# Performance work log

Hardware: AMD Instinct MI355X
Metric: run time of the kernel (lower is better)

## Reference

```python
import jax, jax.numpy as jnp
import numpy as np

C = 256   # embedding_dim
B = 16
N = 2048
BN_EPS = 1e-5


def _sa_params(key, c):
    ks = jax.random.split(key, 8)
    s = 1.0 / np.sqrt(c)
    return dict(
        Wq=jax.random.normal(ks[0], (c // 2, c), jnp.float32) * s,
        Wk=jax.random.normal(ks[1], (c // 2, c), jnp.float32) * s,
        Wv=jax.random.normal(ks[2], (c, c), jnp.float32) * s,
        bv=jax.random.normal(ks[3], (c,), jnp.float32) * 0.01,
        Wt=jax.random.normal(ks[4], (c, c), jnp.float32) * s,
        bt=jax.random.normal(ks[5], (c,), jnp.float32) * 0.01,
        gamma=jnp.ones((c,), jnp.float32),
        beta=jnp.zeros((c,), jnp.float32),
    )


def setup_inputs() -> dict:
    key = jax.random.key(0)
    kx, k1, k2 = jax.random.split(key, 3)
    inp = {"x": jax.random.normal(kx, (B, C, N), jnp.float32)}
    for tag, kk in (("1", k1), ("2", k2)):
        for name, v in _sa_params(kk, C).items():
            inp[name + tag] = v
    return inp


def _sa_layer(x, Wq, Wk, Wv, bv, Wt, bt, gamma, beta):
    # 1x1 conv == per-point linear: [B,C,N]
    x_q = jnp.einsum('oc,bcn->bno', Wq, x)            # [B,N,C/2]
    x_k = jnp.einsum('oc,bcn->bon', Wk, x)            # [B,C/2,N]
    x_v = jnp.einsum('oc,bcn->bon', Wv, x) + bv[None, :, None]
    energy = jnp.einsum('bnc,bcm->bnm', x_q, x_k)     # [B,N,N]
    attn = jax.nn.softmax(energy, axis=-1)
    # offset-attention column-wise L1 renorm
    attn = attn / (1e-9 + attn.sum(axis=1, keepdims=True))
    x_r = jnp.einsum('bcn,bnm->bcm', x_v, attn)       # [B,C,N]
    h = x - x_r
    h = jnp.einsum('oc,bcn->bon', Wt, h) + bt[None, :, None]
    # BatchNorm1d (training mode, biased var over batch+points per channel)
    mean = h.mean(axis=(0, 2), keepdims=True)
    var = jnp.mean((h - mean) ** 2, axis=(0, 2), keepdims=True)
    h = (h - mean) * jax.lax.rsqrt(var + BN_EPS)
    h = h * gamma[None, :, None] + beta[None, :, None]
    return x + jax.nn.relu(h)


def reference(x,
              Wq1, Wk1, Wv1, bv1, Wt1, bt1, gamma1, beta1,
              Wq2, Wk2, Wv2, bv2, Wt2, bt2, gamma2, beta2):
    x1 = _sa_layer(x, Wq1, Wk1, Wv1, bv1, Wt1, bt1, gamma1, beta1)
    x2 = _sa_layer(x1, Wq2, Wk2, Wv2, bv2, Wt2, bt2, gamma2, beta2)
    return jnp.concatenate((x1, x2), axis=1)          # [B,2C,N]
```

## Files before the change

kernel.cpp:

```cpp
#include <hip/hip_runtime.h>

#define DI __device__ __forceinline__

typedef _Float16 f16_t;
typedef _Float16 f16x8 __attribute__((ext_vector_type(8)));
typedef float    f32x4 __attribute__((ext_vector_type(4)));

static_assert(sizeof(f16x8) == 16, "f16x8 must be 16B");

#define B_  16
#define C_  256
#define CH_ 128
#define N_  2048

DI f32x4 fzero(){ f32x4 z = {0.f,0.f,0.f,0.f}; return z; }
DI f16x8 ldg8(const f16_t* p){ return *(const f16x8*)p; }
DI f32x4 mfma16(f16x8 a, f16x8 b, f32x4 c){
  return __builtin_amdgcn_mfma_f32_16x16x32_f16(a, b, c, 0, 0, 0);
}
DI void split2(float v, f16_t& hi, f16_t& lo){
  hi = (f16_t)v; lo = (f16_t)(v - (float)hi);
}
DI int swz_b(int i){ return ((i&7)<<1) | ((i>>3)&1); }

#define GLL16(src, dst) __builtin_amdgcn_global_load_lds( \
    (const __attribute__((address_space(1))) void*)(src), \
    (__attribute__((address_space(3))) void*)(dst), 16, 0, 0)

__global__ void k_wconv(const float* q1,const float* k1,const float* v1,const float* t1,
                        const float* q2,const float* k2,const float* v2,const float* t2,
                        f16_t* out){
  int i = blockIdx.x*256 + threadIdx.x;
  int l = (i >= 196608) ? 1 : 0;
  int r = i - l*196608;
  const float* s; long dbase;
  if(r < 32768){ s = l? q2:q1; dbase = 0; }
  else if(r < 65536){ r -= 32768; s = l? k2:k1; dbase = 65536; }
  else if(r < 131072){ r -= 65536; s = l? v2:v1; dbase = 131072; }
  else { r -= 131072; s = l? t2:t1; dbase = 262144; }
  int o = r >> 8, c = r & 255;
  float v = s[o*256 + c];
  f16_t hi, lo; split2(v, hi, lo);
  f16_t* d = out + (long)l*393216 + dbase + (long)o*512;
  d[c] = hi; d[c+256] = lo;
}

__global__ void k_transpose(const float* __restrict__ X, long bstride,
                            f16_t* __restrict__ XtS){
  int b = blockIdx.x, n0 = blockIdx.y*32, c0 = blockIdx.z*64;
  __shared__ float tl[32][65];
  int t = threadIdx.x;
  int nn = t & 31, cr = t >> 5;
  const float* src = X + (long)b*bstride + n0 + nn;
  #pragma unroll
  for(int i=0;i<8;i++){
    int cc = cr + i*8;
    tl[nn][cc] = src[(long)(c0+cc)*N_];
  }
  __syncthreads();
  int n2 = t >> 3, cq = (t & 7)*8;
  __align__(16) f16_t hi8[8], lo8[8];
  #pragma unroll
  for(int j=0;j<8;j++) split2(tl[n2][cq+j], hi8[j], lo8[j]);
  f16_t* dst = XtS + ((long)b*N_ + n0 + n2)*512 + c0 + cq;
  *(f16x8*)dst         = *(f16x8*)hi8;
  *(f16x8*)(dst + 256) = *(f16x8*)lo8;
}

template<int LGX, int SPLIT_OUT, int BIAS, int DUAL>
__global__ __launch_bounds__(256) void k_gemm3(
    const f16_t* __restrict__ A, long sA,
    const f16_t* __restrict__ Bt, long sB,
    f16_t* __restrict__ out, int ldo, long sO,
    const float* __restrict__ bias, long dualoff)
{
  int i = blockIdx.x;
  int b = swz_b(i);
  int r = i>>4;
  int m0 = (r & ((1<<LGX)-1))*64, n0 = (r >> LGX)*64;
  int t = threadIdx.x, w = t>>6, l = t&63, lr = l&15, lg = l>>4;
  const f16_t* Ab = A + (long)b*sA + (long)(m0 + w*16 + lr)*512;
  const f16_t* Bb = Bt + (long)b*sB;
  f32x4 acc[4];
  #pragma unroll
  for(int i2=0;i2<4;i2++) acc[i2] = fzero();
  for(int k=0;k<256;k+=32){
    f16x8 ah = ldg8(Ab + k + lg*8);
    f16x8 al = ldg8(Ab + 256 + k + lg*8);
    #pragma unroll
    for(int ns=0;ns<4;ns++){
      const f16_t* brow = Bb + (long)(n0 + ns*16 + lr)*512;
      f16x8 bh = ldg8(brow + k + lg*8);
      f16x8 bl = ldg8(brow + 256 + k + lg*8);
      acc[ns] = mfma16(ah, bh, acc[ns]);
      acc[ns] = mfma16(ah, bl, acc[ns]);
      acc[ns] = mfma16(al, bh, acc[ns]);
    }
  }
  f16_t* ob = out + (long)b*sO;
  #pragma unroll
  for(int ns=0;ns<4;ns++){
    #pragma unroll
    for(int j=0;j<4;j++){
      int row = m0 + w*16 + lg*4 + j;
      int col = n0 + ns*16 + lr;
      float v = acc[ns][j];
      if(BIAS) v += bias[row];
      if(SPLIT_OUT){
        f16_t hi, lo; split2(v, hi, lo);
        f16_t* base = ob;
        if(DUAL && col >= 128) base = ob + (dualoff - 128);
        base[(long)row*ldo + col]       = hi;
        base[(long)row*ldo + col + 128] = lo;
      } else {
        ob[(long)row*ldo + col] = (f16_t)v;
      }
    }
  }
}

template<int T3>
__global__ __launch_bounds__(512) void k_rowstats(
    const f16_t* __restrict__ xqS, const f16_t* __restrict__ xkS,
    float* __restrict__ rowoff)
{
  extern __shared__ __align__(16) char smem[];
  const int bi = blockIdx.x;
  const int b = swz_b(bi);
  const int n0 = (bi>>4)*128;
  const int t = threadIdx.x, w = t>>6, l = t&63, lr = l&15, lg = l>>4;

  const f16_t* qp = xqS + ((long)b*N_ + n0 + w*16 + lr)*256;
  f16x8 bqh[4], bql[4];
  #pragma unroll
  for(int k=0;k<4;k++){
    bqh[k] = ldg8(qp + k*32 + lg*8);
    bql[k] = ldg8(qp + 128 + k*32 + lg*8);
  }
  const f16_t* kb = xkS + (long)b*N_*256;

  const int krow_off = l>>5, kslot = l&31;
  const f16_t *ks0, *ks1;
  { int row0 = w*2 + krow_off;
    ks0 = kb + (long)row0*256 + ((kslot ^ (row0&15))*8);
    int row1 = 16 + w*2 + krow_off;
    ks1 = kb + (long)row1*256 + ((kslot ^ (row1&15))*8); }

  #define KSTAGE(buf) do { char* kd = smem + (buf)*16384;                     \
    GLL16(ks0, kd + w*1024); GLL16(ks1, kd + 8192 + w*1024); } while(0)

  float rmax = -3e38f, rsum = 0.f;
  KSTAGE(0);

  #pragma unroll 1
  for(int i=0; i<64; i++){
    const int cur = i&1, nxt = cur^1;
    if(i<63){
      ks0 += 8192; ks1 += 8192;
      KSTAGE(nxt);
      asm volatile("s_waitcnt vmcnt(2)" ::: "memory");
    } else {
      asm volatile("s_waitcnt vmcnt(0)" ::: "memory");
    }
    asm volatile("s_barrier" ::: "memory");
    const char* kbuf = smem + cur*16384;
    #pragma unroll
    for(int s=0;s<2;s++){
      const char* krow = kbuf + (s*16 + lr)*512;
      f16x8 ah[4];
      #pragma unroll
      for(int k=0;k<4;k++)
        ah[k] = *(const f16x8*)(krow + ((((4*k+lg) ^ lr))<<4));
      f32x4 a1 = fzero(), a2 = fzero(), a3 = fzero();
      #pragma unroll
      for(int k=0;k<4;k++) a1 = mfma16(ah[k],  bqh[k], a1);
      #pragma unroll
      for(int k=0;k<4;k++) a2 = mfma16(ah[k],  bql[k], a2);
      if(T3){
        #pragma unroll
        for(int k=0;k<4;k++){
          f16x8 alk = *(const f16x8*)(krow + ((16 + (((4*k+lg)) ^ lr))<<4));
          a3 = mfma16(alk, bqh[k], a3);
        }
      }
      f32x4 acc = (a1 + a2) + a3;
      float vm = fmaxf(fmaxf(acc[0],acc[1]), fmaxf(acc[2],acc[3]));
      float nm = fmaxf(rmax, vm);
      rsum = rsum*__expf(rmax-nm)
           + __expf(acc[0]-nm)+__expf(acc[1]-nm)+__expf(acc[2]-nm)+__expf(acc[3]-nm);
      rmax = nm;
    }
    asm volatile("s_barrier" ::: "memory");
  }
  #undef KSTAGE

  #pragma unroll
  for(int off=16; off<64; off<<=1){
    float om = __shfl_xor(rmax, off, 64);
    float os = __shfl_xor(rsum, off, 64);
    float nm = fmaxf(rmax, om);
    rsum = rsum*__expf(rmax-nm) + os*__expf(om-nm);
    rmax = nm;
  }
  if(lg==0) rowoff[(long)b*N_ + n0 + w*16 + lr] = rmax + __logf(rsum);
}

__global__ __launch_bounds__(256) void k_apply(
    const f16_t* __restrict__ xqS, const f16_t* __restrict__ xkS,
    const f16_t* __restrict__ xv, const float* __restrict__ rowoff,
    const float* __restrict__ X, long xbstride, f16_t* __restrict__ h0T)
{
  extern __shared__ __align__(16) char smem[];
  const int bi = blockIdx.x;
  const int b = swz_b(bi);
  const int m0 = (bi>>4)*64;
  const int t = threadIdx.x, w = t>>6, l = t&63, lr = l&15, lg = l>>4;
  float* ro_s = (float*)(smem + 65536);
  {
    const float* rob = rowoff + (long)b*N_;
    *(f32x4*)(ro_s + t*4)        = *(const f32x4*)(rob + t*4);
    *(f32x4*)(ro_s + t*4 + 1024) = *(const f32x4*)(rob + t*4 + 1024);
  }

  const f16_t* akp = xkS + ((long)b*N_ + m0 + w*16 + lr)*256;
  f16x8 akh[4], akl[4];
  #pragma unroll
  for(int k=0;k<4;k++){
    akh[k] = ldg8(akp + k*32 + lg*8);
    akl[k] = ldg8(akp + 128 + k*32 + lg*8);
  }

  const f16_t* xqb = xqS + (long)b*N_*256;
  const f16_t* xvb = xv + (long)b*C_*N_;
  const int qperm = ((lr>>2)*8 + (lr&3));

  const int qrow_off = (l>>5), qslot = l&31;
  const int vc_off = (l>>2), vslot = l&3;

  const f16_t *qs0,*qs1,*qs2,*qs3,*vs0,*vs1,*vs2,*vs3;
  #define PINIT(r) { int qrow=(r*4+w)*2+qrow_off;                             \
    int qsw=(qrow&3)|(((qrow>>3)&3)<<2);                                      \
    qs##r = xqb + (long)qrow*256 + ((qslot ^ qsw)*8);                         \
    int vc=(r*4+w)*16+vc_off;                                                 \
    vs##r = xvb + (long)vc*N_ + ((vslot ^ (vc&3))*8); }
  PINIT(0) PINIT(1) PINIT(2) PINIT(3)
  #undef PINIT
  #define STAGE(buf) do {                                                     \
    char* qd = smem + (buf)*16384;                                            \
    char* vd = smem + 32768 + (buf)*16384;                                    \
    GLL16(qs0, qd + (0*4+w)*1024); GLL16(vs0, vd + (0*4+w)*1024);             \
    GLL16(qs1, qd + (1*4+w)*1024); GLL16(vs1, vd + (1*4+w)*1024);             \
    GLL16(qs2, qd + (2*4+w)*1024); GLL16(vs2, vd + (2*4+w)*1024);             \
    GLL16(qs3, qd + (3*4+w)*1024); GLL16(vs3, vd + (3*4+w)*1024); } while(0)
  #define PADV() do { qs0+=8192; qs1+=8192; qs2+=8192; qs3+=8192;             \
    vs0+=32; vs1+=32; vs2+=32; vs3+=32; } while(0)

  f32x4 y[16];
  #pragma unroll
  for(int i2=0;i2<16;i2++) y[i2] = fzero();
  float cs = 0.f, cm = -3e38f;

  __syncthreads();
  STAGE(0);

  const int vsl = (lg ^ (lr&3)) << 4;

  #pragma unroll 1
  for(int i=0; i<64; i++){
    const int cur = i&1, nxt = cur^1;
    const int n0 = i*32;
    if(i<63){
      PADV();
      STAGE(nxt);
      asm volatile("s_waitcnt vmcnt(8)" ::: "memory");
    } else {
      asm volatile("s_waitcnt vmcnt(0)" ::: "memory");
    }
    asm volatile("s_barrier" ::: "memory");
    const char* qb = smem + cur*16384;
    const char* vb = smem + 32768 + cur*16384;
    float g[2][4];
    #pragma unroll
    for(int s2=0;s2<2;s2++){
      const int rl = qperm + s2*4;
      const char* qrow = qb + rl*512;
      f16x8 qh[4], ql[4];
      #pragma unroll
      for(int k=0;k<4;k++){
        qh[k] = *(const f16x8*)(qrow + (((4*k + lg) ^ lr)<<4));
        ql[k] = *(const f16x8*)(qrow + 256 + (((4*k + lg) ^ lr)<<4));
      }
      f32x4 e1 = fzero(), e2 = fzero(), e3 = fzero();
      #pragma unroll
      for(int k=0;k<4;k++) e1 = mfma16(qh[k], akh[k], e1);
      #pragma unroll
      for(int k=0;k<4;k++) e2 = mfma16(ql[k], akh[k], e2);
      #pragma unroll
      for(int k=0;k<4;k++) e3 = mfma16(qh[k], akl[k], e3);
      f32x4 e = (e1 + e2) + e3;
      f32x4 ro4 = *(const f32x4*)(ro_s + n0 + lg*8 + s2*4);
      #pragma unroll
      for(int j=0;j<4;j++) g[s2][j] = e[j] - ro4[j];
    }
    float vl = fmaxf(fmaxf(fmaxf(g[0][0],g[0][1]), fmaxf(g[0][2],g[0][3])),
                     fmaxf(fmaxf(g[1][0],g[1][1]), fmaxf(g[1][2],g[1][3])));
    if(__any(vl > cm + 8.f)){
      float v = vl;
      v = fmaxf(v, __shfl_xor(v, 16, 64));
      v = fmaxf(v, __shfl_xor(v, 32, 64));
      bool need = v > cm + 8.f;
      if(need){
        float fj = __expf(cm - v);
        cm = v;
        cs *= fj;
        #pragma unroll
        for(int cf=0;cf<16;cf++){
          #pragma unroll
          for(int j2=0;j2<4;j2++) y[cf][j2] *= fj;
        }
      }
    }
    __align__(16) f16_t pv[8];
    #pragma unroll
    for(int s2=0;s2<2;s2++){
      #pragma unroll
      for(int j=0;j<4;j++){
        float p = __expf(g[s2][j] - cm);
        f16_t pb = (f16_t)p;
        cs += (float)pb;
        pv[s2*4+j] = pb;
      }
    }
    f16x8 pfrag = *(const f16x8*)pv;
    #pragma unroll
    for(int cf=0;cf<16;cf++){
      f16x8 av = *(const f16x8*)(vb + (cf*16 + lr)*64 + vsl);
      y[cf] = mfma16(av, pfrag, y[cf]);
    }
    asm volatile("s_barrier" ::: "memory");
  }
  #undef STAGE
  #undef PADV

  cs += __shfl_xor(cs, 16, 64);
  cs += __shfl_xor(cs, 32, 64);
  float inv = 1.f/(1e-9f*__expf(-cm) + cs);

  f16_t* H = (f16_t*)(smem + 49152);
  const int mq = t&63, cq = t>>6;
  const float* Xb = X + (long)b*xbstride + m0;
  uint4* dstb = (uint4*)(h0T + ((long)b*N_ + m0)*C_);
  #pragma unroll
  for(int half=0; half<2; half++){
    #pragma unroll
    for(int cf8=0; cf8<8; cf8++){
      int cf = half*8 + cf8;
      #pragma unroll
      for(int j=0;j<4;j++){
        int cl = cf8*16 + lg*4 + j;
        int m  = w*16 + lr;
        *(f16_t*)((char*)H + m*256 + ((((cl>>3) ^ (m&7))<<4) | ((cl&7)<<1)))
          = (f16_t)(y[cf][j]*inv);
      }
    }
    __syncthreads();
    #pragma unroll 4
    for(int ci=0; ci<32; ci++){
      int cl = cq*32 + ci;
      int c  = half*128 + cl;
      f16_t* hp = (f16_t*)((char*)H + mq*256 + ((((cl>>3) ^ (mq&7))<<4) | ((cl&7)<<1)));
      *hp = (f16_t)(Xb[(long)c*N_ + mq] - (float)*hp);
    }
    __syncthreads();
    {
      const uint4* src = (const uint4*)H;
      for(int i2=t;i2<1024;i2+=256){
        int row = i2>>4, slot = i2&15;
        dstb[row*32 + half*16 + slot] = src[(i2 & ~15) | (slot ^ (row&7))];
      }
    }
    __syncthreads();
  }
}

__global__ __launch_bounds__(256) void k_wt_bn(
    const f16_t* __restrict__ WtS, const f16_t* __restrict__ h0T,
    const float* __restrict__ bt,
    f16_t* __restrict__ h1, float* __restrict__ bnacc)
{
  int i = blockIdx.x;
  int b = swz_b(i);
  int r = i>>4;
  int o0 = (r&3)*64, m0 = (r>>2)*64;
  int t=threadIdx.x, w=t>>6, l=t&63, lr=l&15, lg=l>>4;
  const f16_t* Arow = WtS + (long)(o0 + w*16 + lr)*512;
  const f16_t* Bb = h0T + (long)b*N_*C_;
  f32x4 acc[4];
  #pragma unroll
  for(int i2=0;i2<4;i2++) acc[i2] = fzero();
  for(int k=0;k<C_;k+=32){
    f16x8 afh = ldg8(Arow + k + lg*8);
    f16x8 afl = ldg8(Arow + 256 + k + lg*8);
    #pragma unroll
    for(int ms=0;ms<4;ms++){
      f16x8 bf_ = ldg8(Bb + (long)(m0 + ms*16 + lr)*C_ + k + lg*8);
      acc[ms] = mfma16(afh, bf_, acc[ms]);
      acc[ms] = mfma16(afl, bf_, acc[ms]);
    }
  }
  float s1[4]={0.f,0.f,0.f,0.f}, s2v[4]={0.f,0.f,0.f,0.f};
  f16_t* h1b = h1 + (long)b*C_*N_;
  #pragma unroll
  for(int j=0;j<4;j++){
    int o = o0 + w*16 + lg*4 + j;
    float bias = bt[o];
    #pragma unroll
    for(int ms=0;ms<4;ms++){
      float v = acc[ms][j] + bias;
      h1b[(long)o*N_ + m0 + ms*16 + lr] = (f16_t)v;
      s1[j] += v; s2v[j] += v*v;
    }
  }
  #pragma unroll
  for(int off=1; off<16; off<<=1){
    #pragma unroll
    for(int j=0;j<4;j++){ s1[j]+=__shfl_xor(s1[j],off,64); s2v[j]+=__shfl_xor(s2v[j],off,64); }
  }
  if(lr==0){
    #pragma unroll
    for(int j=0;j<4;j++){
      int o = o0 + w*16 + lg*4 + j;
      atomicAdd(&bnacc[o], s1[j]);
      atomicAdd(&bnacc[256+o], s2v[j]);
    }
  }
}

__global__ void k_out(const f16_t* __restrict__ h1, const float* __restrict__ X, long xbstride,
                      const float* __restrict__ bnacc, const float* __restrict__ gamma,
                      const float* __restrict__ beta, float* __restrict__ out, long ocoff){
  long i = (long)blockIdx.x*256 + threadIdx.x;
  long e = i*8;
  int b = (int)(e >> 19);
  int rem = (int)(e & 524287);
  int c = rem >> 11;
  float mean = bnacc[c] * (1.f/32768.f);
  float var  = bnacc[256+c] * (1.f/32768.f) - mean*mean;
  float sc = gamma[c] * rsqrtf(var + 1e-5f);
  float sh = beta[c] - mean*sc;
  f16x8 hv = *(const f16x8*)(h1 + e);
  const float* xb = X + (long)b*xbstride + rem;
  float4 xr0 = *(const float4*)xb;
  float4 xr1 = *(const float4*)(xb + 4);
  float4 o0, o1;
  o0.x = xr0.x + fmaxf(fmaf((float)hv[0], sc, sh), 0.f);
  o0.y = xr0.y + fmaxf(fmaf((float)hv[1], sc, sh), 0.f);
  o0.z = xr0.z + fmaxf(fmaf((float)hv[2], sc, sh), 0.f);
  o0.w = xr0.w + fmaxf(fmaf((float)hv[3], sc, sh), 0.f);
  o1.x = xr1.x + fmaxf(fmaf((float)hv[4], sc, sh), 0.f);
  o1.y = xr1.y + fmaxf(fmaf((float)hv[5], sc, sh), 0.f);
  o1.z = xr1.z + fmaxf(fmaf((float)hv[6], sc, sh), 0.f);
  o1.w = xr1.w + fmaxf(fmaf((float)hv[7], sc, sh), 0.f);
  float* ob = out + (long)b*(512L*N_) + ocoff + rem;
  *(float4*)ob       = o0;
  *(float4*)(ob + 4) = o1;
}

extern "C" void kernel_launch(void* const* d_in, const int* in_sizes, int n_in,
                              void* d_out, int out_size, void* d_ws, size_t ws_size,
                              hipStream_t stream){
  (void)in_sizes; (void)n_in; (void)out_size; (void)ws_size;
  const float* x = (const float*)d_in[0];
  const float *Wf[2][4], *bv[2], *bt[2], *gm[2], *bb[2];
  for(int l=0;l<2;l++){
    int base = 1 + l*8;
    Wf[l][0]=(const float*)d_in[base+0];
    Wf[l][1]=(const float*)d_in[base+1];
    Wf[l][2]=(const float*)d_in[base+2];
    bv[l]   =(const float*)d_in[base+3];
    Wf[l][3]=(const float*)d_in[base+4];
    bt[l]   =(const float*)d_in[base+5];
    gm[l]   =(const float*)d_in[base+6];
    bb[l]   =(const float*)d_in[base+7];
  }
  char* ws = (char*)d_ws;
  size_t off = 0;
  auto alloc = [&](size_t bytes){ size_t o = off; off += (bytes + 255) & ~(size_t)255; return o; };
  size_t oXt = alloc((size_t)B_*N_*512*2);
  size_t oXq = alloc((size_t)B_*N_*256*2);
  size_t oXk = alloc((size_t)B_*N_*256*2);
  size_t oXv = alloc((size_t)B_*C_*N_*2);
  size_t oH0 = alloc((size_t)B_*N_*C_*2);
  size_t oRo = alloc((size_t)B_*N_*4);
  size_t oBn = alloc(2*512*4);
  size_t oW  = alloc((size_t)786432*2);

  hipMemsetAsync(ws + oBn, 0, 2*512*4, stream);
  k_wconv<<<1536,256,0,stream>>>(Wf[0][0],Wf[0][1],Wf[0][2],Wf[0][3],
                                 Wf[1][0],Wf[1][1],Wf[1][2],Wf[1][3],
                                 (f16_t*)(ws+oW));
  float* dout = (float*)d_out;
  f16_t* H1 = (f16_t*)(ws + oXq);
  const long XKOFF = ((long)(oXk - oXq)) / 2;
  for(int l=0;l<2;l++){
    const float* Xl = l ? dout : x;
    long xbs = l ? 512L*N_ : 256L*N_;
    const f16_t* WqS = (const f16_t*)(ws+oW) + (size_t)l*393216;
    const f16_t* WvS = WqS + 131072;
    const f16_t* WtS = WqS + 262144;
    f16_t* XtS = (f16_t*)(ws+oXt);
    f16_t* Xq  = (f16_t*)(ws+oXq);
    f16_t* Xk  = (f16_t*)(ws+oXk);
    f16_t* Xv  = (f16_t*)(ws+oXv);
    f16_t* H0  = (f16_t*)(ws+oH0);
    float* Ro  = (float*)(ws+oRo);
    float* Bn  = (float*)(ws+oBn) + l*512;

    k_transpose<<<dim3(B_, N_/32, C_/64),256,0,stream>>>(Xl, xbs, XtS);
    k_gemm3<5,1,0,1><<<2048,256,0,stream>>>(XtS, (long)N_*512, WqS, 0L,
                                            Xq, 256, (long)N_*256, nullptr, XKOFF);
    k_gemm3<2,0,1,0><<<2048,256,0,stream>>>(WvS, 0L, XtS, (long)N_*512,
                                            Xv, N_, (long)C_*N_, bv[l], 0L);
    if(l==0) k_rowstats<1><<<256,512,32768,stream>>>(Xq, Xk, Ro);
    else     k_rowstats<0><<<256,512,32768,stream>>>(Xq, Xk, Ro);
    k_apply<<<512,256,73728,stream>>>(Xq, Xk, Xv, Ro, Xl, xbs, H0);
    k_wt_bn<<<2048,256,0,stream>>>(WtS, H0, bt[l], H1, Bn);
    k_out<<<4096,256,0,stream>>>(H1, Xl, xbs, Bn, gm[l], bb[l], dout, (long)l*C_*N_);
  }
}
```

Before: 856.8 us.

## Double k_apply block to 512 threads covering 128 columns to share staged Q/V tiles

k_apply now runs 512-thread blocks, each handling 128 output columns instead of 64, with half as many blocks. The per-iteration Q and V tiles staged into shared memory are shared by eight waves instead of four, so each thread issues fewer global-to-LDS loads. Global traffic for the repeated xq/xv streams per batch drops by half. In exchange, the grid shrinks to 256 blocks, which lowers the number of independent blocks available to fill the GPU. The epilogue buffer is moved to a different LDS offset to fit the larger H tile.

```diff
diff --git a/kernel.cpp b/kernel.cpp
--- a/kernel.cpp
+++ b/kernel.cpp
@@ -205,7 +205,7 @@
   if(lg==0) rowoff[(long)b*N_ + n0 + w*16 + lr] = rmax + __logf(rsum);
 }
 
-__global__ __launch_bounds__(256) void k_apply(
+__global__ __launch_bounds__(512) void k_apply(
     const f16_t* __restrict__ xqS, const f16_t* __restrict__ xkS,
     const f16_t* __restrict__ xv, const float* __restrict__ rowoff,
     const float* __restrict__ X, long xbstride, f16_t* __restrict__ h0T)
@@ -213,13 +213,12 @@
   extern __shared__ __align__(16) char smem[];
   const int bi = blockIdx.x;
   const int b = swz_b(bi);
-  const int m0 = (bi>>4)*64;
+  const int m0 = (bi>>4)*128;
   const int t = threadIdx.x, w = t>>6, l = t&63, lr = l&15, lg = l>>4;
   float* ro_s = (float*)(smem + 65536);
   {
     const float* rob = rowoff + (long)b*N_;
-    *(f32x4*)(ro_s + t*4)        = *(const f32x4*)(rob + t*4);
-    *(f32x4*)(ro_s + t*4 + 1024) = *(const f32x4*)(rob + t*4 + 1024);
+    *(f32x4*)(ro_s + t*4) = *(const f32x4*)(rob + t*4);
   }
 
   const f16_t* akp = xkS + ((long)b*N_ + m0 + w*16 + lr)*256;
@@ -237,23 +236,20 @@
   const int qrow_off = (l>>5), qslot = l&31;
   const int vc_off = (l>>2), vslot = l&3;
 
-  const f16_t *qs0,*qs1,*qs2,*qs3,*vs0,*vs1,*vs2,*vs3;
-  #define PINIT(r) { int qrow=(r*4+w)*2+qrow_off;                             \
-    int qsw=(qrow&3)|(((qrow>>3)&3)<<2);                                      \
-    qs##r = xqb + (long)qrow*256 + ((qslot ^ qsw)*8);                         \
-    int vc=(r*4+w)*16+vc_off;                                                 \
-    vs##r = xvb + (long)vc*N_ + ((vslot ^ (vc&3))*8); }
-  PINIT(0) PINIT(1) PINIT(2) PINIT(3)
-  #undef PINIT
-  #define STAGE(buf) do {                                                     \
+  #define STAGE(nn, buf) do {                                                 \
     char* qd = smem + (buf)*16384;                                            \
     char* vd = smem + 32768 + (buf)*16384;                                    \
-    GLL16(qs0, qd + (0*4+w)*1024); GLL16(vs0, vd + (0*4+w)*1024);             \
-    GLL16(qs1, qd + (1*4+w)*1024); GLL16(vs1, vd + (1*4+w)*1024);             \
-    GLL16(qs2, qd + (2*4+w)*1024); GLL16(vs2, vd + (2*4+w)*1024);             \
-    GLL16(qs3, qd + (3*4+w)*1024); GLL16(vs3, vd + (3*4+w)*1024); } while(0)
-  #define PADV() do { qs0+=8192; qs1+=8192; qs2+=8192; qs3+=8192;             \
-    vs0+=32; vs1+=32; vs2+=32; vs3+=32; } while(0)
+    _Pragma("unroll")                                                         \
+    for(int r=0;r<2;r++){                                                     \
+      int qrow = (r*8+w)*2 + qrow_off;                                        \
+      int qsw  = (qrow&3) | (((qrow>>3)&3)<<2);                               \
+      const f16_t* qsrc = xqb + (long)((nn) + qrow)*256 + ((qslot ^ qsw)*8);  \
+      GLL16(qsrc, qd + (r*8+w)*1024);                                         \
+      int vc = (r*8+w)*16 + vc_off;                                           \
+      const f16_t* vsrc2 = xvb + (long)vc*N_ + (nn) + ((vslot ^ (vc&3))*8);   \
+      GLL16(vsrc2, vd + (r*8+w)*1024);                                        \
+    }                                                                         \
+  } while(0)
 
   f32x4 y[16];
   #pragma unroll
@@ -261,7 +257,7 @@
   float cs = 0.f, cm = -3e38f;
 
   __syncthreads();
-  STAGE(0);
+  STAGE(0, 0);
 
   const int vsl = (lg ^ (lr&3)) << 4;
 
@@ -270,9 +266,8 @@
     const int cur = i&1, nxt = cur^1;
     const int n0 = i*32;
     if(i<63){
-      PADV();
-      STAGE(nxt);
-      asm volatile("s_waitcnt vmcnt(8)" ::: "memory");
+      STAGE(n0+32, nxt);
+      asm volatile("s_waitcnt vmcnt(4)" ::: "memory");
     } else {
       asm volatile("s_waitcnt vmcnt(0)" ::: "memory");
     }
@@ -340,14 +335,13 @@
     asm volatile("s_barrier" ::: "memory");
   }
   #undef STAGE
-  #undef PADV
 
   cs += __shfl_xor(cs, 16, 64);
   cs += __shfl_xor(cs, 32, 64);
   float inv = 1.f/(1e-9f*__expf(-cm) + cs);
 
-  f16_t* H = (f16_t*)(smem + 49152);
-  const int mq = t&63, cq = t>>6;
+  f16_t* H = (f16_t*)(smem + 32768);
+  const int mq = t&127, cq = t>>7;
   const float* Xb = X + (long)b*xbstride + m0;
   uint4* dstb = (uint4*)(h0T + ((long)b*N_ + m0)*C_);
   #pragma unroll
@@ -374,7 +368,7 @@
     __syncthreads();
     {
       const uint4* src = (const uint4*)H;
-      for(int i2=t;i2<1024;i2+=256){
+      for(int i2=t;i2<2048;i2+=512){
         int row = i2>>4, slot = i2&15;
         dstb[row*32 + half*16 + slot] = src[(i2 & ~15) | (slot ^ (row&7))];
       }
@@ -523,7 +517,7 @@
                                             Xv, N_, (long)C_*N_, bv[l], 0L);
     if(l==0) k_rowstats<1><<<256,512,32768,stream>>>(Xq, Xk, Ro);
     else     k_rowstats<0><<<256,512,32768,stream>>>(Xq, Xk, Ro);
-    k_apply<<<512,256,73728,stream>>>(Xq, Xk, Xv, Ro, Xl, xbs, H0);
+    k_apply<<<256,512,73728,stream>>>(Xq, Xk, Xv, Ro, Xl, xbs, H0);
     k_wt_bn<<<2048,256,0,stream>>>(WtS, H0, bt[l], H1, Bn);
     k_out<<<4096,256,0,stream>>>(H1, Xl, xbs, Bn, gm[l], bb[l], dout, (long)l*C_*N_);
   }
```

After: 819.6 us. 1.05x faster.
